# Kernel optimization log

Measured on AMD Instinct MI355X. Metric: run time of the kernel, lower is better.

## Reference

```python
import jax, jax.numpy as jnp
import numpy as np

B, G1, S, GS, D, T, H = 64, 128, 32, 16, 384, 10, 6
HD = D // H
SCALE = HD ** -0.5
GELU = lambda v: jax.nn.gelu(v, approximate=False)


def layer_norm(v, g, b, eps=1e-5):
    m = jnp.mean(v, -1, keepdims=True)
    s = jnp.mean((v - m) ** 2, -1, keepdims=True)
    return (v - m) * jax.lax.rsqrt(s + eps) * g + b


def mha(xn, qkv_w, proj_w, proj_b):
    Bc, N, C = xn.shape
    qkv = (xn @ qkv_w.T).reshape(Bc, N, 3, H, HD)
    qkv = jnp.transpose(qkv, (2, 0, 3, 1, 4))  # [3,B,H,N,hd]
    q, k, v = qkv[0], qkv[1], qkv[2]
    attn = jax.nn.softmax(jnp.einsum('bhnd,bhmd->bhnm', q, k) * SCALE, axis=-1)
    o = jnp.einsum('bhnm,bhmd->bhnd', attn, v)
    o = jnp.transpose(o, (0, 2, 1, 3)).reshape(Bc, N, C)
    return o @ proj_w.T + proj_b, attn


def propagate(xyz1, xyz2, points1, points2, de_neighbors):
    # squared pairwise distances [B,N,S]
    d = jnp.sum((xyz1[:, :, None, :] - xyz2[:, None, :, :]) ** 2, -1)
    order = jnp.argsort(d, axis=-1)[..., :de_neighbors]
    dists = jnp.take_along_axis(d, order, axis=-1)
    w = 1.0 / (dists + 1e-8)
    w = w / jnp.sum(w, -1, keepdims=True)
    gathered = jax.vmap(lambda p, i: p[i])(points2, order)  # [B,N,de,Dp]
    interp = jnp.sum(gathered * w[..., None], axis=2)
    return points1 + 0.3 * interp


def setup_inputs() -> dict:
    key = jax.random.key(0)
    ks = iter(jax.random.split(key, 64))
    rn = lambda sh, sc=1.0: jax.random.normal(next(ks), sh, jnp.float32) * sc
    w = 0.02
    inp = dict(
        x=rn((B, G1 + 1, D)),
        mask=jnp.zeros((B, G1, G1), jnp.float32),
        center1=rn((B, G1, 3)),
        center2=rn((B, S, 3)),
        neighborhood=rn((B, S, GS, 3)),
        idx=jax.random.randint(next(ks), (B * S * GS,), 0, B * (G1 + T)),
        center_idx=jax.random.randint(next(ks), (B * S,), 0, B * (G1 + T)),
        group_size=GS,
        layer_id=3,
        ln1_g=jnp.ones((D,)), ln1_b=jnp.zeros((D,)),
        ln2_g=jnp.ones((D,)), ln2_b=jnp.zeros((D,)),
        qkv_w=rn((3 * D, D), w), proj_w=rn((D, D), w), proj_b=jnp.zeros((D,)),
        fc1_w=rn((4 * D, D), w), fc1_b=jnp.zeros((4 * D,)),
        fc2_w=rn((D, 4 * D), w), fc2_b=jnp.zeros((D,)),
        ad_down_w=rn((16, D), w), ad_down_b=jnp.zeros((16,)),
        ad_up_w=rn((D, 16), w), ad_up_b=jnp.zeros((D,)),
        ad1_down_w=rn((16, D), w), ad1_down_b=jnp.zeros((16,)),
        ad1_up_w=rn((D, 16), w), ad1_up_b=jnp.zeros((D,)),
        prompt_emb=rn((T, D), w),
        bn_g=jnp.ones((D,)), bn_b=jnp.zeros((D,)),
        bn_mean=jnp.zeros((D,)), bn_var=jnp.ones((D,)),
        qkv1_w=rn((3 * D, D), w), proj1_w=rn((D, D), w), proj1_b=jnp.zeros((D,)),
        ln3_g=jnp.ones((D,)), ln3_b=jnp.zeros((D,)),
    )
    return inp


def block_forward(x, mask, center1, center2, neighborhood, idx, center_idx,
                  group_size, layer_id,
                  ln1_g, ln1_b, ln2_g, ln2_b, qkv_w, proj_w, proj_b,
                  fc1_w, fc1_b, fc2_w, fc2_b,
                  ad_down_w, ad_down_b, ad_up_w, ad_up_b,
                  ad1_down_w, ad1_down_b, ad1_up_w, ad1_up_b,
                  prompt_emb, bn_g, bn_b, bn_mean, bn_var,
                  qkv1_w, proj1_w, proj1_b, ln3_g, ln3_b):
    Bc = x.shape[0]
    # mask padding (built but unused by Attention, matching the source)
    # layer_id <= 5 branch (layer_id=3)
    prompt = jnp.broadcast_to(prompt_emb[None], (Bc, T, D))  # dropout off (eval)
    x = jnp.concatenate([x[:, :1], prompt, x[:, 1:]], axis=1)  # [B, 1+T+G1, D]
    x_fn, attn_weight = mha(layer_norm(x, ln1_g, ln1_b), qkv_w, proj_w, proj_b)
    x = x_fn + x
    xn2 = layer_norm(x, ln2_g, ln2_b)
    x_fn = GELU(xn2 @ fc1_w.T + fc1_b) @ fc2_w.T + fc2_b
    # AdapterSuper_f: bottleneck down-GELU-up (no internal residual)
    ad = GELU(x_fn @ ad_down_w.T + ad_down_b) @ ad_up_w.T + ad_up_b
    x = 0.7 * ad + x_fn + x
    prompt = x[:, 1:T + 1]
    x = jnp.concatenate([x[:, :1], x[:, T + 1:]], axis=1)  # [B, 1+G1, D]
    cls_x = x[:, 0]
    x = x[:, 1:]  # [B, G1, D]
    G = G1 + T
    prompt_x = jnp.concatenate([prompt, x], axis=1).reshape(Bc * G, D)
    x_neigh = prompt_x[idx].reshape(Bc * S, group_size, D)
    x_centers = prompt_x[center_idx].reshape(Bc, S, D)
    _ = neighborhood / (jnp.std(neighborhood) + 1e-5)  # dead in source
    # local attention over each neighborhood group
    xn3 = layer_norm(x_neigh, ln3_g, ln3_b)
    attn1_out, _a = mha(xn3, qkv1_w, proj1_w, proj1_b)
    x_neigh = attn1_out + x_neigh
    # pooling: max over group, then eval BatchNorm1d + GELU over channel dim
    lc = jnp.max(x_neigh.reshape(Bc, S, group_size, D), axis=2)  # [B,S,D]
    lc = (lc - bn_mean) * jax.lax.rsqrt(bn_var + 1e-5) * bn_g + bn_b
    lc = GELU(lc)
    vis_x = lc + 0.3 * x_centers
    x = propagate(center1, center2, x, vis_x, S)
    x = jnp.concatenate([cls_x[:, None], prompt, x], axis=1)  # [B, 1+T+G1, D]
    # AdapterSuper: bottleneck with internal residual
    x = GELU(x @ ad1_down_w.T + ad1_down_b) @ ad1_up_w.T + ad1_up_b + x
    x = jnp.concatenate([x[:, :1], x[:, T + 1:]], axis=1)  # [B, 1+G1, D]
    return x, attn_weight


def reference(x, mask, center1, center2, neighborhood, idx, center_idx,
              group_size, layer_id,
              ln1_g, ln1_b, ln2_g, ln2_b, qkv_w, proj_w, proj_b,
              fc1_w, fc1_b, fc2_w, fc2_b,
              ad_down_w, ad_down_b, ad_up_w, ad_up_b,
              ad1_down_w, ad1_down_b, ad1_up_w, ad1_up_b,
              prompt_emb, bn_g, bn_b, bn_mean, bn_var,
              qkv1_w, proj1_w, proj1_b, ln3_g, ln3_b):
    return block_forward(x, mask, center1, center2, neighborhood, idx, center_idx,
                         group_size, layer_id,
                         ln1_g, ln1_b, ln2_g, ln2_b, qkv_w, proj_w, proj_b,
                         fc1_w, fc1_b, fc2_w, fc2_b,
                         ad_down_w, ad_down_b, ad_up_w, ad_up_b,
                         ad1_down_w, ad1_down_b, ad1_up_w, ad1_up_b,
                         prompt_emb, bn_g, bn_b, bn_mean, bn_var,
                         qkv1_w, proj1_w, proj1_b, ln3_g, ln3_b)
```

## Files before the change

### kernel.cpp

```cpp
#include <hip/hip_runtime.h>
#include <hip/hip_bf16.h>

typedef __hip_bfloat16 bf16;
typedef __attribute__((ext_vector_type(8))) short short8;
typedef __attribute__((ext_vector_type(4))) float f32x4;

#define DEV static __device__ __forceinline__

DEV float b2f(bf16 v) { return __bfloat162float(v); }
DEV bf16 f2b(float v) { return __float2bfloat16(v); }
DEV unsigned short f2bu(float v) { return __builtin_bit_cast(unsigned short, __float2bfloat16(v)); }
DEV float u2f(unsigned short u) { return __uint_as_float(((unsigned int)u) << 16); }
DEV float gelu(float x) { return 0.5f * x * (1.0f + erff(x * 0.70710678118654752f)); }

#define BB 64
#define NT 139
#define DD 384
#define TT 10
#define HH 6
#define GG 138
#define M1 8896
#define MG 8832
#define NGRP 2048
#define SCALE 0.125f

#define XC_OFF   0UL
#define VIS_OFF  13664256UL
#define XNB_OFF  16809984UL
#define XFN_OFF  23642112UL
#define T16_OFF  37306368UL
#define BIG1_OFF 37875712UL
#define BIG2_OFF 58372096UL
#define ATT_OFF  XNB_OFF
#define WB_OFF   85700608UL

#define WB_QKV   0
#define WB_PROJ  442368
#define WB_FC1   589824
#define WB_FC2   1179648
#define WB_QKV1  1769472
#define WB_PROJ1 2211840
#define WB_TOTAL 2359296

#define OUT_X 3170304

DEV float4 ld4(const float* p) { return *(const float4*)p; }
DEV float4 ld4(const bf16* p) {
    ushort4 u = *(const ushort4*)p;
    return make_float4(u2f(u.x), u2f(u.y), u2f(u.z), u2f(u.w));
}
DEV void stc(float* p, float v) { *p = v; }
DEV void stc(bf16* p, float v) { *p = f2b(v); }

__global__ __launch_bounds__(256) void k_wconv(const float* __restrict__ w0, const float* __restrict__ w1,
                                               const float* __restrict__ w2, const float* __restrict__ w3,
                                               const float* __restrict__ w4, const float* __restrict__ w5,
                                               bf16* __restrict__ dst) {
    int i4 = (blockIdx.x * 256 + threadIdx.x) * 4;
    if (i4 >= WB_TOTAL) return;
    const float* s; int off;
    if (i4 < WB_PROJ)       { s = w0; off = WB_QKV; }
    else if (i4 < WB_FC1)   { s = w1; off = WB_PROJ; }
    else if (i4 < WB_FC2)   { s = w2; off = WB_FC1; }
    else if (i4 < WB_QKV1)  { s = w3; off = WB_FC2; }
    else if (i4 < WB_PROJ1) { s = w4; off = WB_QKV1; }
    else                    { s = w5; off = WB_PROJ1; }
    float4 v = *(const float4*)(s + (i4 - off));
    ushort4 u;
    u.x = f2bu(v.x); u.y = f2bu(v.y); u.z = f2bu(v.z); u.w = f2bu(v.w);
    *(ushort4*)((unsigned short*)dst + i4) = u;
}

__global__ __launch_bounds__(256) void k_build_xc(const float* __restrict__ x,
                                                  const float* __restrict__ pe,
                                                  float* __restrict__ xc) {
    int i = blockIdx.x * 256 + threadIdx.x;
    if (i >= M1 * DD) return;
    int d = i % DD, r = i / DD, n = r % NT, b = r / NT;
    float v;
    if (n == 0)        v = x[(b * 129) * DD + d];
    else if (n <= TT)  v = pe[(n - 1) * DD + d];
    else               v = x[(b * 129 + n - TT) * DD + d];
    xc[i] = v;
}

__global__ __launch_bounds__(128) void k_layernorm(const float* __restrict__ src, bf16* __restrict__ dst,
                                                   const float* __restrict__ g, const float* __restrict__ bta,
                                                   int mode) {
    int r = blockIdx.x;
    int srow = r;
    if (mode) srow = (r / GG) * NT + 1 + (r % GG);
    const float* p = src + (size_t)srow * DD;
    int t = threadIdx.x;
    float v0 = p[t], v1 = p[t + 128], v2 = p[t + 256];
    __shared__ float red[4];
    float s = v0 + v1 + v2;
    for (int off = 32; off; off >>= 1) s += __shfl_down(s, off, 64);
    if ((t & 63) == 0) red[t >> 6] = s;
    __syncthreads();
    float mean = (red[0] + red[1]) * (1.0f / 384.0f);
    float d0 = v0 - mean, d1 = v1 - mean, d2 = v2 - mean;
    float s2 = d0 * d0 + d1 * d1 + d2 * d2;
    for (int off = 32; off; off >>= 1) s2 += __shfl_down(s2, off, 64);
    if ((t & 63) == 0) red[2 + (t >> 6)] = s2;
    __syncthreads();
    float rstd = rsqrtf((red[2] + red[3]) * (1.0f / 384.0f) + 1e-5f);
    bf16* q = dst + (size_t)r * DD;
    q[t]       = f2b(d0 * rstd * g[t]       + bta[t]);
    q[t + 128] = f2b(d1 * rstd * g[t + 128] + bta[t + 128]);
    q[t + 256] = f2b(d2 * rstd * g[t + 256] + bta[t + 256]);
}

template <typename TC>
__global__ __launch_bounds__(256) void mf_gemm(const bf16* __restrict__ A, const bf16* __restrict__ W,
                                               const float* __restrict__ bias, const float* __restrict__ res,
                                               TC* __restrict__ C, int M, int N, int K, int act) {
    __shared__ bf16 As[128][40];
    __shared__ bf16 Ws[64][40];
    int t = threadIdx.x;
    int m0 = blockIdx.y * 128, n0 = blockIdx.x * 64;
    int lane = t & 63, wv = t >> 6;
    int wm = (wv >> 1) * 64, wn = (wv & 1) * 32;
    int fr = lane & 15, fq = lane >> 4;
    int sr = t >> 2, sc = (t & 3) * 8;
    f32x4 acc[4][2] = {};
    for (int k0 = 0; k0 < K; k0 += 32) {
        int gr = m0 + sr; if (gr >= M) gr = M - 1;
        *(uint4*)&As[sr][sc] = *(const uint4*)(A + (size_t)gr * K + k0 + sc);
        int gr2 = m0 + 64 + sr; if (gr2 >= M) gr2 = M - 1;
        *(uint4*)&As[64 + sr][sc] = *(const uint4*)(A + (size_t)gr2 * K + k0 + sc);
        *(uint4*)&Ws[sr][sc] = *(const uint4*)(W + (size_t)(n0 + sr) * K + k0 + sc);
        __syncthreads();
        short8 af[4], bfr[2];
#pragma unroll
        for (int i = 0; i < 4; ++i) af[i] = *(const short8*)&As[wm + i * 16 + fr][fq * 8];
#pragma unroll
        for (int j = 0; j < 2; ++j) bfr[j] = *(const short8*)&Ws[wn + j * 16 + fr][fq * 8];
#pragma unroll
        for (int i = 0; i < 4; ++i)
#pragma unroll
            for (int j = 0; j < 2; ++j)
                acc[i][j] = __builtin_amdgcn_mfma_f32_16x16x32_bf16(af[i], bfr[j], acc[i][j], 0, 0, 0);
        __syncthreads();
    }
#pragma unroll
    for (int i = 0; i < 4; ++i) {
#pragma unroll
        for (int r = 0; r < 4; ++r) {
            int row = m0 + wm + i * 16 + fq * 4 + r;
            if (row < M) {
                size_t ro = (size_t)row * N;
#pragma unroll
                for (int j = 0; j < 2; ++j) {
                    int col = n0 + wn + j * 16 + fr;
                    float c = acc[i][j][r];
                    if (bias) c += bias[col];
                    if (act == 1) c = gelu(c);
                    if (res) c += res[ro + col];
                    stc(&C[ro + col], c);
                }
            }
        }
    }
}

#define BM 64
#define BN 64
#define BKK 16
template <typename TA, typename TC>
__global__ __launch_bounds__(256) void k_gemm(const TA* __restrict__ A, const float* __restrict__ W,
                                              const float* __restrict__ bias, const float* __restrict__ res,
                                              TC* __restrict__ C, int M, int N, int K, int act) {
    __shared__ float As[BKK][BM + 4];
    __shared__ float Wsm[BKK][BN + 4];
    int t = threadIdx.x;
    int tx = t & 15, ty = t >> 4;
    int m0 = blockIdx.y * BM, n0 = blockIdx.x * BN;
    int lr = t >> 2;
    int lk = (t & 3) * 4;
    float acc[4][4] = {};
    for (int k0 = 0; k0 < K; k0 += BKK) {
        float4 av = ld4(A + (size_t)(m0 + lr) * K + k0 + lk);
        As[lk + 0][lr] = av.x; As[lk + 1][lr] = av.y;
        As[lk + 2][lr] = av.z; As[lk + 3][lr] = av.w;
        int wrr = n0 + lr;
        float4 wv = make_float4(0.f, 0.f, 0.f, 0.f);
        if (wrr < N) wv = ld4(W + (size_t)wrr * K + k0 + lk);
        Wsm[lk + 0][lr] = wv.x; Wsm[lk + 1][lr] = wv.y;
        Wsm[lk + 2][lr] = wv.z; Wsm[lk + 3][lr] = wv.w;
        __syncthreads();
#pragma unroll
        for (int k = 0; k < BKK; ++k) {
            float a0 = As[k][ty * 4 + 0], a1 = As[k][ty * 4 + 1];
            float a2 = As[k][ty * 4 + 2], a3 = As[k][ty * 4 + 3];
            float b0 = Wsm[k][tx * 4 + 0], b1 = Wsm[k][tx * 4 + 1];
            float b2 = Wsm[k][tx * 4 + 2], b3 = Wsm[k][tx * 4 + 3];
            acc[0][0] += a0 * b0; acc[0][1] += a0 * b1; acc[0][2] += a0 * b2; acc[0][3] += a0 * b3;
            acc[1][0] += a1 * b0; acc[1][1] += a1 * b1; acc[1][2] += a1 * b2; acc[1][3] += a1 * b3;
            acc[2][0] += a2 * b0; acc[2][1] += a2 * b1; acc[2][2] += a2 * b2; acc[2][3] += a2 * b3;
            acc[3][0] += a3 * b0; acc[3][1] += a3 * b1; acc[3][2] += a3 * b2; acc[3][3] += a3 * b3;
        }
        __syncthreads();
    }
#pragma unroll
    for (int i = 0; i < 4; ++i) {
        int m = m0 + ty * 4 + i;
        size_t ro = (size_t)m * N;
#pragma unroll
        for (int j = 0; j < 4; ++j) {
            int n = n0 + tx * 4 + j;
            if (n < N) {
                float c = acc[i][j];
                if (bias) c += bias[n];
                if (act == 1) c = gelu(c);
                if (res) c += res[ro + n];
                stc(&C[ro + n], c);
            }
        }
    }
}

__global__ __launch_bounds__(256) void k_attn1(const bf16* __restrict__ qkv, bf16* __restrict__ o_out,
                                               float* __restrict__ attn_out) {
    int bh = blockIdx.x;
    int b = bh / HH, h = bh % HH;
    __shared__ unsigned short Kl[144][72];
    __shared__ unsigned short Vt[64][160];
    __shared__ unsigned short Pl[4][16][160];
    int t = threadIdx.x;
    int lane = t & 63, wv = t >> 6;
    int fr = lane & 15, fq = lane >> 4;
    const unsigned short* q16 = (const unsigned short*)qkv;
    size_t base = (size_t)b * NT * 1152;

    uint4 z4 = make_uint4(0, 0, 0, 0);
    for (int i = t * 8; i < 64 * 160; i += 2048) *(uint4*)(&Vt[0][0] + i) = z4;
    for (int i = t * 8; i < 4 * 16 * 160; i += 2048) *(uint4*)(&Pl[0][0][0] + i) = z4;
    for (int i = t; i < 144 * 8; i += 256) {
        int row = i >> 3, ch = (i & 7) * 8;
        uint4 v = z4;
        if (row < NT) v = *(const uint4*)(q16 + base + row * 1152 + 384 + h * 64 + ch);
        *(uint4*)&Kl[row][ch] = v;
    }
    for (int i = t; i < NT * 16; i += 256) {
        int m = i >> 4, dq = (i & 15) * 4;
        ushort4 v = *(const ushort4*)(q16 + base + m * 1152 + 768 + h * 64 + dq);
        Vt[dq + 0][m] = v.x; Vt[dq + 1][m] = v.y;
        Vt[dq + 2][m] = v.z; Vt[dq + 3][m] = v.w;
    }
    __syncthreads();

    for (int nt = wv; nt < 9; nt += 4) {
        int n0 = nt * 16;
        int arow = n0 + fr; if (arow > NT - 1) arow = NT - 1;
        const unsigned short* qp = q16 + base + (size_t)arow * 1152 + h * 64 + fq * 8;
        short8 a0 = *(const short8*)qp;
        short8 a1 = *(const short8*)(qp + 32);
        f32x4 s[9] = {};
#pragma unroll
        for (int mt = 0; mt < 9; ++mt) {
            short8 b0 = *(const short8*)&Kl[mt * 16 + fr][fq * 8];
            short8 b1 = *(const short8*)&Kl[mt * 16 + fr][32 + fq * 8];
            s[mt] = __builtin_amdgcn_mfma_f32_16x16x32_bf16(a0, b0, s[mt], 0, 0, 0);
            s[mt] = __builtin_amdgcn_mfma_f32_16x16x32_bf16(a1, b1, s[mt], 0, 0, 0);
        }
#pragma unroll
        for (int r = 0; r < 4; ++r) {
            float e[9];
            float mx = -1e30f;
#pragma unroll
            for (int mt = 0; mt < 9; ++mt) {
                int col = mt * 16 + fr;
                float v = (col < NT) ? s[mt][r] * SCALE : -1e30f;
                e[mt] = v;
                mx = fmaxf(mx, v);
            }
#pragma unroll
            for (int off = 1; off < 16; off <<= 1) mx = fmaxf(mx, __shfl_xor(mx, off, 64));
            float sm = 0.f;
#pragma unroll
            for (int mt = 0; mt < 9; ++mt) { e[mt] = __expf(e[mt] - mx); sm += e[mt]; }
#pragma unroll
            for (int off = 1; off < 16; off <<= 1) sm += __shfl_xor(sm, off, 64);
            float inv = 1.0f / sm;
            int n = n0 + fq * 4 + r;
            bool nv = n < NT;
            size_t ab = ((size_t)(b * HH + h) * NT + n) * NT;
#pragma unroll
            for (int mt = 0; mt < 9; ++mt) {
                float p = e[mt] * inv;
                int col = mt * 16 + fr;
                if (nv && col < NT) attn_out[ab + col] = p;
                Pl[wv][fq * 4 + r][col] = f2bu(p);
            }
        }
        __syncthreads();
        f32x4 oac[4] = {};
#pragma unroll
        for (int ks = 0; ks < 5; ++ks) {
            short8 ap = *(const short8*)&Pl[wv][fr][ks * 32 + fq * 8];
#pragma unroll
            for (int dt = 0; dt < 4; ++dt) {
                short8 bv = *(const short8*)&Vt[dt * 16 + fr][ks * 32 + fq * 8];
                oac[dt] = __builtin_amdgcn_mfma_f32_16x16x32_bf16(ap, bv, oac[dt], 0, 0, 0);
            }
        }
#pragma unroll
        for (int dt = 0; dt < 4; ++dt)
#pragma unroll
            for (int r = 0; r < 4; ++r) {
                int n = n0 + fq * 4 + r;
                if (n < NT)
                    o_out[((size_t)(b * NT + n)) * DD + h * 64 + dt * 16 + fr] = f2b(oac[dt][r]);
            }
    }
}

__global__ __launch_bounds__(64) void k_attn2(const bf16* __restrict__ qkv, const int* __restrict__ idx,
                                              bf16* __restrict__ o1) {
    int g = blockIdx.x;
    __shared__ unsigned short Vt2[64][40];
    __shared__ unsigned short P2[16][40];
    __shared__ int ridx[16];
    int t = threadIdx.x;
    int fr = t & 15, fq = t >> 4;
    const unsigned short* q16 = (const unsigned short*)qkv;
    if (t < 16) ridx[t] = idx[g * 16 + t];
    uint4 z4 = make_uint4(0, 0, 0, 0);
    for (int i = t * 8; i < 64 * 40; i += 512) *(uint4*)(&Vt2[0][0] + i) = z4;
    for (int i = t * 8; i < 16 * 40; i += 512) *(uint4*)(&P2[0][0] + i) = z4;
    __syncthreads();
    size_t qb = (size_t)ridx[fr] * 1152;
    for (int h = 0; h < HH; ++h) {
        for (int i = t; i < 256; i += 64) {
            int m = i >> 4, dq = (i & 15) * 4;
            ushort4 v = *(const ushort4*)(q16 + (size_t)ridx[m] * 1152 + 768 + h * 64 + dq);
            Vt2[dq + 0][m] = v.x; Vt2[dq + 1][m] = v.y;
            Vt2[dq + 2][m] = v.z; Vt2[dq + 3][m] = v.w;
        }
        __syncthreads();
        const unsigned short* qp = q16 + qb + h * 64 + fq * 8;
        const unsigned short* kp = q16 + qb + 384 + h * 64 + fq * 8;
        short8 a0 = *(const short8*)qp;
        short8 a1 = *(const short8*)(qp + 32);
        short8 b0 = *(const short8*)kp;
        short8 b1 = *(const short8*)(kp + 32);
        f32x4 s = {};
        s = __builtin_amdgcn_mfma_f32_16x16x32_bf16(a0, b0, s, 0, 0, 0);
        s = __builtin_amdgcn_mfma_f32_16x16x32_bf16(a1, b1, s, 0, 0, 0);
#pragma unroll
        for (int r = 0; r < 4; ++r) {
            float v = s[r] * SCALE;
            float mx = v;
#pragma unroll
            for (int off = 1; off < 16; off <<= 1) mx = fmaxf(mx, __shfl_xor(mx, off, 64));
            float e = __expf(v - mx), sm = e;
#pragma unroll
            for (int off = 1; off < 16; off <<= 1) sm += __shfl_xor(sm, off, 64);
            P2[fq * 4 + r][fr] = f2bu(e / sm);
        }
        __syncthreads();
        short8 ap = *(const short8*)&P2[fr][fq * 8];
        f32x4 oac[4] = {};
#pragma unroll
        for (int dt = 0; dt < 4; ++dt) {
            short8 bv = *(const short8*)&Vt2[dt * 16 + fr][fq * 8];
            oac[dt] = __builtin_amdgcn_mfma_f32_16x16x32_bf16(ap, bv, oac[dt], 0, 0, 0);
        }
#pragma unroll
        for (int dt = 0; dt < 4; ++dt)
#pragma unroll
            for (int r = 0; r < 4; ++r)
                o1[((size_t)(g * 16 + fq * 4 + r)) * DD + h * 64 + dt * 16 + fr] = f2b(oac[dt][r]);
        __syncthreads();
    }
}

__global__ __launch_bounds__(128) void k_ad_combine(const float* __restrict__ t16, const float* __restrict__ upw,
                                                    const float* __restrict__ upb, const float* __restrict__ xfn,
                                                    float* xc) {
    int r = blockIdx.x, t = threadIdx.x;
    __shared__ float tl[16];
    if (t < 16) tl[t] = t16[r * 16 + t];
    __syncthreads();
    for (int d = t; d < DD; d += 128) {
        float acc = 0.f;
#pragma unroll
        for (int c = 0; c < 4; ++c) {
            float4 u = *(const float4*)(upw + d * 16 + c * 4);
            acc += tl[c * 4 + 0] * u.x + tl[c * 4 + 1] * u.y
                 + tl[c * 4 + 2] * u.z + tl[c * 4 + 3] * u.w;
        }
        acc += upb[d];
        size_t i = (size_t)r * DD + d;
        xc[i] += 0.7f * acc + xfn[i];
    }
}

__global__ __launch_bounds__(128) void k_groupmax(const bf16* __restrict__ att, const float* __restrict__ xc,
                                                  const int* __restrict__ idx, const int* __restrict__ cidx,
                                                  const float* __restrict__ bg, const float* __restrict__ bb,
                                                  const float* __restrict__ bmean, const float* __restrict__ bvar,
                                                  float* __restrict__ vis) {
    int g = blockIdx.x, t = threadIdx.x;
    __shared__ int rows[16];
    __shared__ int crow;
    if (t < 16) { int r = idx[g * 16 + t]; rows[t] = (r / GG) * NT + 1 + (r % GG); }
    if (t == 16) { int r = cidx[g]; crow = (r / GG) * NT + 1 + (r % GG); }
    __syncthreads();
    for (int d = t; d < DD; d += 128) {
        float m = -INFINITY;
#pragma unroll
        for (int j = 0; j < 16; ++j) {
            float v = b2f(att[((size_t)(g * 16 + j)) * DD + d]) + xc[(size_t)rows[j] * DD + d];
            m = fmaxf(m, v);
        }
        float bn = (m - bmean[d]) * rsqrtf(bvar[d] + 1e-5f) * bg[d] + bb[d];
        bn = gelu(bn);
        vis[(size_t)g * DD + d] = bn + 0.3f * xc[(size_t)crow * DD + d];
    }
}

__global__ __launch_bounds__(128) void k_propagate(const float* __restrict__ c1, const float* __restrict__ c2,
                                                   const float* __restrict__ xc, const float* __restrict__ vis,
                                                   float* __restrict__ xp) {
    int blk = blockIdx.x;
    int b = blk >> 7, i = blk & 127;
    int t = threadIdx.x;
    __shared__ float wl[32];
    __shared__ float wsum;
    if (t < 32) {
        float dx = c1[(b * 128 + i) * 3 + 0] - c2[(b * 32 + t) * 3 + 0];
        float dy = c1[(b * 128 + i) * 3 + 1] - c2[(b * 32 + t) * 3 + 1];
        float dz = c1[(b * 128 + i) * 3 + 2] - c2[(b * 32 + t) * 3 + 2];
        wl[t] = 1.0f / (dx * dx + dy * dy + dz * dz + 1e-8f);
    }
    __syncthreads();
    if (t == 0) {
        float s = 0.f;
        for (int j = 0; j < 32; ++j) s += wl[j];
        wsum = s;
    }
    __syncthreads();
    float sc = 0.3f / wsum;
    for (int d = t; d < DD; d += 128) {
        float acc = 0.f;
#pragma unroll 8
        for (int j = 0; j < 32; ++j) acc += wl[j] * vis[((size_t)(b * 32 + j)) * DD + d];
        xp[((size_t)(b * 128 + i)) * DD + d] = xc[((size_t)(b * NT + 11 + i)) * DD + d] + sc * acc;
    }
}

__global__ __launch_bounds__(256) void k_build_xfinal(const float* __restrict__ xc, const float* __restrict__ xp,
                                                      float* __restrict__ xf) {
    int i = blockIdx.x * 256 + threadIdx.x;
    if (i >= M1 * DD) return;
    int d = i % DD, r = i / DD, n = r % NT, b = r / NT;
    xf[i] = (n < 11) ? xc[i] : xp[((size_t)(b * 128 + n - 11)) * DD + d];
}

__global__ __launch_bounds__(128) void k_final(const float* __restrict__ t16, const float* __restrict__ upw,
                                               const float* __restrict__ upb, const float* __restrict__ xf,
                                               float* __restrict__ outx) {
    int rb = blockIdx.x, t = threadIdx.x;
    int b = rb / 129, no = rb % 129;
    int src = b * NT + (no == 0 ? 0 : no + TT);
    __shared__ float tl[16];
    if (t < 16) tl[t] = t16[src * 16 + t];
    __syncthreads();
    for (int d = t; d < DD; d += 128) {
        float acc = 0.f;
#pragma unroll
        for (int c = 0; c < 4; ++c) {
            float4 u = *(const float4*)(upw + d * 16 + c * 4);
            acc += tl[c * 4 + 0] * u.x + tl[c * 4 + 1] * u.y
                 + tl[c * 4 + 2] * u.z + tl[c * 4 + 3] * u.w;
        }
        acc += upb[d];
        outx[(size_t)rb * DD + d] = acc + xf[(size_t)src * DD + d];
    }
}

extern "C" void kernel_launch(void* const* d_in, const int* in_sizes, int n_in,
                              void* d_out, int out_size, void* d_ws, size_t ws_size,
                              hipStream_t stream) {
    const float* x_in    = (const float*)d_in[0];
    const float* center1 = (const float*)d_in[2];
    const float* center2 = (const float*)d_in[3];
    const int*   idx     = (const int*)d_in[5];
    const int*   cidx    = (const int*)d_in[6];
    const float* ln1_g   = (const float*)d_in[9];
    const float* ln1_b   = (const float*)d_in[10];
    const float* ln2_g   = (const float*)d_in[11];
    const float* ln2_b   = (const float*)d_in[12];
    const float* qkv_w   = (const float*)d_in[13];
    const float* proj_w  = (const float*)d_in[14];
    const float* proj_b  = (const float*)d_in[15];
    const float* fc1_w   = (const float*)d_in[16];
    const float* fc1_b   = (const float*)d_in[17];
    const float* fc2_w   = (const float*)d_in[18];
    const float* fc2_b   = (const float*)d_in[19];
    const float* ad_dw   = (const float*)d_in[20];
    const float* ad_db   = (const float*)d_in[21];
    const float* ad_uw   = (const float*)d_in[22];
    const float* ad_ub   = (const float*)d_in[23];
    const float* ad1_dw  = (const float*)d_in[24];
    const float* ad1_db  = (const float*)d_in[25];
    const float* ad1_uw  = (const float*)d_in[26];
    const float* ad1_ub  = (const float*)d_in[27];
    const float* prompt  = (const float*)d_in[28];
    const float* bn_g    = (const float*)d_in[29];
    const float* bn_b    = (const float*)d_in[30];
    const float* bn_mean = (const float*)d_in[31];
    const float* bn_var  = (const float*)d_in[32];
    const float* qkv1_w  = (const float*)d_in[33];
    const float* proj1_w = (const float*)d_in[34];
    const float* proj1_b = (const float*)d_in[35];
    const float* ln3_g   = (const float*)d_in[36];
    const float* ln3_b   = (const float*)d_in[37];

    char* wsb = (char*)d_ws;
    float* XC   = (float*)(wsb + XC_OFF);
    float* VIS  = (float*)(wsb + VIS_OFF);
    bf16*  XNB  = (bf16*)(wsb + XNB_OFF);
    float* XFN  = (float*)(wsb + XFN_OFF);
    float* T16  = (float*)(wsb + T16_OFF);
    bf16*  BIG1 = (bf16*)(wsb + BIG1_OFF);
    bf16*  BIG2 = (bf16*)(wsb + BIG2_OFF);
    float* XFIN = (float*)(wsb + BIG2_OFF);
    bf16*  ATT  = (bf16*)(wsb + ATT_OFF);
    bf16*  WB   = (bf16*)(wsb + WB_OFF);

    float* out_x    = (float*)d_out;
    float* out_attn = out_x + OUT_X;

    k_wconv<<<(WB_TOTAL / 4 + 255) / 256, 256, 0, stream>>>(qkv_w, proj_w, fc1_w, fc2_w, qkv1_w, proj1_w, WB);

    k_build_xc<<<(M1 * DD + 255) / 256, 256, 0, stream>>>(x_in, prompt, XC);
    k_layernorm<<<M1, 128, 0, stream>>>(XC, XNB, ln1_g, ln1_b, 0);
    mf_gemm<<<dim3(18, 70), 256, 0, stream>>>(XNB, WB + WB_QKV, (const float*)nullptr, (const float*)nullptr, BIG1, M1, 1152, 384, 0);
    k_attn1<<<BB * HH, 256, 0, stream>>>(BIG1, XNB, out_attn);
    mf_gemm<<<dim3(6, 70), 256, 0, stream>>>(XNB, WB + WB_PROJ, proj_b, XC, XC, M1, 384, 384, 0);
    k_layernorm<<<M1, 128, 0, stream>>>(XC, XNB, ln2_g, ln2_b, 0);
    mf_gemm<<<dim3(24, 70), 256, 0, stream>>>(XNB, WB + WB_FC1, fc1_b, (const float*)nullptr, BIG2, M1, 1536, 384, 1);
    mf_gemm<<<dim3(6, 70), 256, 0, stream>>>(BIG2, WB + WB_FC2, fc2_b, (const float*)nullptr, XFN, M1, 384, 1536, 0);
    k_gemm<<<dim3(1, 139), 256, 0, stream>>>(XFN, ad_dw, ad_db, (const float*)nullptr, T16, M1, 16, 384, 1);
    k_ad_combine<<<M1, 128, 0, stream>>>(T16, ad_uw, ad_ub, XFN, XC);

    k_layernorm<<<MG, 128, 0, stream>>>(XC, XNB, ln3_g, ln3_b, 1);
    mf_gemm<<<dim3(18, 69), 256, 0, stream>>>(XNB, WB + WB_QKV1, (const float*)nullptr, (const float*)nullptr, BIG1, MG, 1152, 384, 0);
    k_attn2<<<NGRP, 64, 0, stream>>>(BIG1, idx, BIG2);
    mf_gemm<<<dim3(6, 256), 256, 0, stream>>>(BIG2, WB + WB_PROJ1, proj1_b, (const float*)nullptr, ATT, NGRP * 16, 384, 384, 0);
    k_groupmax<<<NGRP, 128, 0, stream>>>(ATT, XC, idx, cidx, bn_g, bn_b, bn_mean, bn_var, VIS);
    k_propagate<<<BB * 128, 128, 0, stream>>>(center1, center2, XC, VIS, XFN);

    k_build_xfinal<<<(M1 * DD + 255) / 256, 256, 0, stream>>>(XC, XFN, XFIN);
    k_gemm<<<dim3(1, 139), 256, 0, stream>>>(XFIN, ad1_dw, ad1_db, (const float*)nullptr, T16, M1, 16, 384, 1);
    k_final<<<BB * 129, 128, 0, stream>>>(T16, ad1_uw, ad1_ub, XFIN, out_x);
}
```

Before: 541.8 us.

## Retile MFMA GEMM to 64x64 with BK=64 and register-prefetched global loads

```diff
diff --git a/kernel.cpp b/kernel.cpp
--- a/kernel.cpp
+++ b/kernel.cpp
@@ -115,50 +115,60 @@
 __global__ __launch_bounds__(256) void mf_gemm(const bf16* __restrict__ A, const bf16* __restrict__ W,
                                                const float* __restrict__ bias, const float* __restrict__ res,
                                                TC* __restrict__ C, int M, int N, int K, int act) {
-    __shared__ bf16 As[128][40];
-    __shared__ bf16 Ws[64][40];
+    __shared__ bf16 As[64][72];
+    __shared__ bf16 Ws[64][72];
     int t = threadIdx.x;
-    int m0 = blockIdx.y * 128, n0 = blockIdx.x * 64;
+    int m0 = blockIdx.y * 64, n0 = blockIdx.x * 64;
     int lane = t & 63, wv = t >> 6;
-    int wm = (wv >> 1) * 64, wn = (wv & 1) * 32;
+    int wm = (wv >> 1) * 32, wn = (wv & 1) * 32;
     int fr = lane & 15, fq = lane >> 4;
-    int sr = t >> 2, sc = (t & 3) * 8;
-    f32x4 acc[4][2] = {};
-    for (int k0 = 0; k0 < K; k0 += 32) {
-        int gr = m0 + sr; if (gr >= M) gr = M - 1;
-        *(uint4*)&As[sr][sc] = *(const uint4*)(A + (size_t)gr * K + k0 + sc);
-        int gr2 = m0 + 64 + sr; if (gr2 >= M) gr2 = M - 1;
-        *(uint4*)&As[64 + sr][sc] = *(const uint4*)(A + (size_t)gr2 * K + k0 + sc);
-        *(uint4*)&Ws[sr][sc] = *(const uint4*)(W + (size_t)(n0 + sr) * K + k0 + sc);
-        __syncthreads();
-        short8 af[4], bfr[2];
-#pragma unroll
-        for (int i = 0; i < 4; ++i) af[i] = *(const short8*)&As[wm + i * 16 + fr][fq * 8];
-#pragma unroll
-        for (int j = 0; j < 2; ++j) bfr[j] = *(const short8*)&Ws[wn + j * 16 + fr][fq * 8];
-#pragma unroll
-        for (int i = 0; i < 4; ++i)
-#pragma unroll
-            for (int j = 0; j < 2; ++j)
-                acc[i][j] = __builtin_amdgcn_mfma_f32_16x16x32_bf16(af[i], bfr[j], acc[i][j], 0, 0, 0);
-        __syncthreads();
-    }
-#pragma unroll
-    for (int i = 0; i < 4; ++i) {
+    int sr = t >> 2, sc = (t & 3) * 16;
+    const bf16* pa = A + (size_t)(m0 + sr) * K + sc;
+    const bf16* pw = W + (size_t)(n0 + sr) * K + sc;
+    uint4 ra0 = *(const uint4*)pa;
+    uint4 ra1 = *(const uint4*)(pa + 8);
+    uint4 rw0 = *(const uint4*)pw;
+    uint4 rw1 = *(const uint4*)(pw + 8);
+    f32x4 acc[2][2] = {};
+    int k0 = 0;
+    for (;;) {
+        *(uint4*)&As[sr][sc] = ra0; *(uint4*)&As[sr][sc + 8] = ra1;
+        *(uint4*)&Ws[sr][sc] = rw0; *(uint4*)&Ws[sr][sc + 8] = rw1;
+        __syncthreads();
+        k0 += 64;
+        bool more = (k0 < K);
+        if (more) {
+            ra0 = *(const uint4*)(pa + k0); ra1 = *(const uint4*)(pa + k0 + 8);
+            rw0 = *(const uint4*)(pw + k0); rw1 = *(const uint4*)(pw + k0 + 8);
+        }
+#pragma unroll
+        for (int ks = 0; ks < 2; ++ks) {
+            short8 a0 = *(const short8*)&As[wm + fr][ks * 32 + fq * 8];
+            short8 a1 = *(const short8*)&As[wm + 16 + fr][ks * 32 + fq * 8];
+            short8 b0 = *(const short8*)&Ws[wn + fr][ks * 32 + fq * 8];
+            short8 b1 = *(const short8*)&Ws[wn + 16 + fr][ks * 32 + fq * 8];
+            acc[0][0] = __builtin_amdgcn_mfma_f32_16x16x32_bf16(a0, b0, acc[0][0], 0, 0, 0);
+            acc[0][1] = __builtin_amdgcn_mfma_f32_16x16x32_bf16(a0, b1, acc[0][1], 0, 0, 0);
+            acc[1][0] = __builtin_amdgcn_mfma_f32_16x16x32_bf16(a1, b0, acc[1][0], 0, 0, 0);
+            acc[1][1] = __builtin_amdgcn_mfma_f32_16x16x32_bf16(a1, b1, acc[1][1], 0, 0, 0);
+        }
+        if (!more) break;
+        __syncthreads();
+    }
+#pragma unroll
+    for (int i = 0; i < 2; ++i) {
 #pragma unroll
         for (int r = 0; r < 4; ++r) {
             int row = m0 + wm + i * 16 + fq * 4 + r;
-            if (row < M) {
-                size_t ro = (size_t)row * N;
-#pragma unroll
-                for (int j = 0; j < 2; ++j) {
-                    int col = n0 + wn + j * 16 + fr;
-                    float c = acc[i][j][r];
-                    if (bias) c += bias[col];
-                    if (act == 1) c = gelu(c);
-                    if (res) c += res[ro + col];
-                    stc(&C[ro + col], c);
-                }
+            size_t ro = (size_t)row * N;
+#pragma unroll
+            for (int j = 0; j < 2; ++j) {
+                int col = n0 + wn + j * 16 + fr;
+                float c = acc[i][j][r];
+                if (bias) c += bias[col];
+                if (act == 1) c = gelu(c);
+                if (res) c += res[ro + col];
+                stc(&C[ro + col], c);
             }
         }
     }
@@ -538,19 +548,19 @@
 
     k_build_xc<<<(M1 * DD + 255) / 256, 256, 0, stream>>>(x_in, prompt, XC);
     k_layernorm<<<M1, 128, 0, stream>>>(XC, XNB, ln1_g, ln1_b, 0);
-    mf_gemm<<<dim3(18, 70), 256, 0, stream>>>(XNB, WB + WB_QKV, (const float*)nullptr, (const float*)nullptr, BIG1, M1, 1152, 384, 0);
+    mf_gemm<<<dim3(18, 139), 256, 0, stream>>>(XNB, WB + WB_QKV, (const float*)nullptr, (const float*)nullptr, BIG1, M1, 1152, 384, 0);
     k_attn1<<<BB * HH, 256, 0, stream>>>(BIG1, XNB, out_attn);
-    mf_gemm<<<dim3(6, 70), 256, 0, stream>>>(XNB, WB + WB_PROJ, proj_b, XC, XC, M1, 384, 384, 0);
+    mf_gemm<<<dim3(6, 139), 256, 0, stream>>>(XNB, WB + WB_PROJ, proj_b, XC, XC, M1, 384, 384, 0);
     k_layernorm<<<M1, 128, 0, stream>>>(XC, XNB, ln2_g, ln2_b, 0);
-    mf_gemm<<<dim3(24, 70), 256, 0, stream>>>(XNB, WB + WB_FC1, fc1_b, (const float*)nullptr, BIG2, M1, 1536, 384, 1);
-    mf_gemm<<<dim3(6, 70), 256, 0, stream>>>(BIG2, WB + WB_FC2, fc2_b, (const float*)nullptr, XFN, M1, 384, 1536, 0);
+    mf_gemm<<<dim3(24, 139), 256, 0, stream>>>(XNB, WB + WB_FC1, fc1_b, (const float*)nullptr, BIG2, M1, 1536, 384, 1);
+    mf_gemm<<<dim3(6, 139), 256, 0, stream>>>(BIG2, WB + WB_FC2, fc2_b, (const float*)nullptr, XFN, M1, 384, 1536, 0);
     k_gemm<<<dim3(1, 139), 256, 0, stream>>>(XFN, ad_dw, ad_db, (const float*)nullptr, T16, M1, 16, 384, 1);
     k_ad_combine<<<M1, 128, 0, stream>>>(T16, ad_uw, ad_ub, XFN, XC);
 
     k_layernorm<<<MG, 128, 0, stream>>>(XC, XNB, ln3_g, ln3_b, 1);
-    mf_gemm<<<dim3(18, 69), 256, 0, stream>>>(XNB, WB + WB_QKV1, (const float*)nullptr, (const float*)nullptr, BIG1, MG, 1152, 384, 0);
+    mf_gemm<<<dim3(18, 138), 256, 0, stream>>>(XNB, WB + WB_QKV1, (const float*)nullptr, (const float*)nullptr, BIG1, MG, 1152, 384, 0);
     k_attn2<<<NGRP, 64, 0, stream>>>(BIG1, idx, BIG2);
-    mf_gemm<<<dim3(6, 256), 256, 0, stream>>>(BIG2, WB + WB_PROJ1, proj1_b, (const float*)nullptr, ATT, NGRP * 16, 384, 384, 0);
+    mf_gemm<<<dim3(6, 512), 256, 0, stream>>>(BIG2, WB + WB_PROJ1, proj1_b, (const float*)nullptr, ATT, NGRP * 16, 384, 384, 0);
     k_groupmax<<<NGRP, 128, 0, stream>>>(ATT, XC, idx, cidx, bn_g, bn_b, bn_mean, bn_var, VIS);
     k_propagate<<<BB * 128, 128, 0, stream>>>(center1, center2, XC, VIS, XFN);
 
```

Measured after the change: 498.6 us. 8.0% less time.
